# Kernel tuning notes

Hardware: AMD Instinct MI355X
Metric: run time of the kernel (lower is better)

The kernel has to match this reference:

```python
import jax, jax.numpy as jnp
import numpy as np

ALPHA = 0.2  # LeakyReLU negative slope
OUT_FEATURES = 64


def setup_inputs() -> dict:
    key = jax.random.key(0)
    k1, k2, k3, k4 = jax.random.split(key, 4)
    n_nodes, n_edges = 50000, 800000
    in_f, out_f, n_heads = 128, OUT_FEATURES, 4
    x = jax.random.normal(k1, (n_nodes, in_f), dtype=jnp.float32)
    edge_index = jax.random.randint(k2, (2, n_edges), 0, n_nodes, dtype=jnp.int64)
    # xavier-ish scaled params
    W = jax.random.normal(k3, (n_heads, in_f, out_f), dtype=jnp.float32) * (1.0 / np.sqrt(in_f))
    a = jax.random.normal(k4, (n_heads, 2 * out_f, 1), dtype=jnp.float32) * (1.0 / np.sqrt(2 * out_f))
    return {"x": x, "edge_index": edge_index, "W": W, "a": a}


def reference(x, edge_index, W, a):
    n_nodes = x.shape[0]
    out_f = W.shape[-1]
    src, dst = edge_index[0], edge_index[1]
    # per-head linear transform: (n, h, o)
    xt = jnp.einsum('ni,hio->nho', x, W)
    x_src = xt[src]  # (e, h, o) - edge-wise gather
    x_dst = xt[dst]
    # split attention vector: concat([x_src, x_dst]) @ a == x_src@a_src + x_dst@a_dst
    a_src = a[:, :out_f, 0]  # (h, o)
    a_dst = a[:, out_f:, 0]
    e = jnp.einsum('eho,ho->eh', x_src, a_src) + jnp.einsum('eho,ho->eh', x_dst, a_dst)
    e = jax.nn.leaky_relu(e, negative_slope=ALPHA)
    # segment softmax over incoming edges of each dst node (all heads at once)
    max_e = jax.ops.segment_max(e, dst, num_segments=n_nodes)  # (n, h), -inf for empty
    max_e = jnp.where(max_e == -jnp.inf, 0.0, max_e)
    exp_e = jnp.exp(e - max_e[dst])
    sum_exp = jax.ops.segment_sum(exp_e, dst, num_segments=n_nodes)
    attention = exp_e / (sum_exp[dst] + 1e-10)  # (e, h)
    # weighted scatter-add aggregation
    weighted = x_src * attention[..., None]  # (e, h, o)
    out = jax.ops.segment_sum(weighted, dst, num_segments=n_nodes)  # (n, h, o)
    out = out.reshape(n_nodes, -1)  # concat heads
    return out
```

## Files before the change

kernel.cpp:

```cpp
#include <hip/hip_runtime.h>
#include <math.h>

constexpr int IN_F  = 128;
constexpr int OUT_F = 64;
constexpr int HEADS = 4;
constexpr int COLS  = HEADS * OUT_F;
constexpr float ALPHA = 0.2f;
constexpr int CAP  = 64;
constexpr int NBUCK = 256;
constexpr int REPL  = 8;
constexpr int CAPBR = 768;
constexpr int CH_A  = 3840;
constexpr float QS   = 7.0f / 127.0f;
constexpr float QINV = 127.0f / 7.0f;

typedef __attribute__((ext_vector_type(8))) short short8v;
typedef __attribute__((ext_vector_type(4))) float f32x4;

__device__ inline unsigned short f2bf(float f) {
  unsigned int u = __float_as_uint(f);
  u += 0x7FFF + ((u >> 16) & 1);
  return (unsigned short)(u >> 16);
}

__device__ inline int wave_incl_scan(int v, int lane) {
  #pragma unroll
  for (int ofs = 1; ofs < 64; ofs <<= 1) {
    int tv = __shfl_up(v, ofs, 64);
    if (lane >= ofs) v += tv;
  }
  return v;
}

__device__ inline void fma8u(float* acc, float p, const uint2 v) {
  acc[0] += p * (float)( v.x        & 0xFF);
  acc[1] += p * (float)((v.x >> 8 ) & 0xFF);
  acc[2] += p * (float)((v.x >> 16) & 0xFF);
  acc[3] += p * (float)( v.x >> 24        );
  acc[4] += p * (float)( v.y        & 0xFF);
  acc[5] += p * (float)((v.y >> 8 ) & 0xFF);
  acc[6] += p * (float)((v.y >> 16) & 0xFF);
  acc[7] += p * (float)( v.y >> 24        );
}

__global__ __launch_bounds__(256) void k_prep(const float* __restrict__ W,
                                              unsigned short* __restrict__ Wb,
                                              int* __restrict__ gcursorR) {
  int i = blockIdx.x * 256 + threadIdx.x;
  if (i < NBUCK * REPL) gcursorR[i] = 0;
  if (i < HEADS * IN_F * OUT_F) {
    int h = i >> 13;
    int o = (i >> 7) & 63;
    int k = i & 127;
    Wb[i] = f2bf(W[(size_t)h * 8192 + k * 64 + o]);
  }
}

__global__ __launch_bounds__(256) void k_big(const float* __restrict__ x,
                                             const unsigned short* __restrict__ Wb,
                                             const float* __restrict__ a,
                                             const int* __restrict__ ei,
                                             unsigned char* __restrict__ xtb8,
                                             float* __restrict__ s_src,
                                             float* __restrict__ s_dst,
                                             int* __restrict__ gcursorR,
                                             unsigned int* __restrict__ gbuf,
                                             int n, int E, int NB_A) {
  __shared__ char smem[19456];
  __shared__ int wt[4];
  const int bid = blockIdx.x;
  const int t = threadIdx.x;
  const int lane = t & 63;
  const int wid = t >> 6;

  if (bid < NB_A) {
    unsigned int* stage = (unsigned int*)smem;
    int* cnt   = (int*)(smem + 15360);
    int* basei = (int*)(smem + 16384);
    int* cur   = (int*)(smem + 17408);
    int* gbase = (int*)(smem + 18432);
    const int rep = bid & (REPL - 1);

    cnt[t] = 0;
    __syncthreads();

    const int e0 = bid * CH_A;
    for (int i = t; i < CH_A; i += 256) {
      int e = e0 + i;
      if (e < E) atomicAdd(&cnt[ei[E + e] >> 8], 1);
    }
    __syncthreads();

    {
      int v = cnt[t];
      int incl = wave_incl_scan(v, lane);
      if (lane == 63) wt[wid] = incl;
      __syncthreads();
      int wofs = 0;
      #pragma unroll
      for (int w = 0; w < 4; ++w) wofs += (w < wid) ? wt[w] : 0;
      basei[t] = wofs + incl - v;
      cur[t] = wofs + incl - v;
    }
    __syncthreads();

    for (int i = t; i < CH_A; i += 256) {
      int e = e0 + i;
      if (e < E) {
        int src = ei[e];
        int dst = ei[E + e];
        int b = dst >> 8;
        int pos = atomicAdd(&cur[b], 1);
        stage[pos] = ((unsigned int)src << 16) | (unsigned int)(dst & 255);
      }
    }
    __syncthreads();

    if (t < NBUCK) {
      int c = cnt[t];
      gbase[t] = c ? atomicAdd(&gcursorR[t * REPL + rep], c) : 0;
    }
    __syncthreads();

    for (int b = wid; b < NBUCK; b += 4) {
      int c = cnt[b];
      int gb = gbase[b];
      int lb = basei[b];
      unsigned int* gdst = gbuf + ((size_t)b * REPL + rep) * CAPBR + gb;
      for (int i = lane; i < c; i += 64)
        gdst[i] = stage[lb + i];
    }
    return;
  }

  unsigned short* xls = (unsigned short*)smem;
  const int rbase = (bid - NB_A) * 64;
  const int w = wid;

  for (int c = t; c < 2048; c += 256) {
    int row = c >> 5;
    int i4  = c & 31;
    int grow = rbase + row;
    float4 v = make_float4(0.f, 0.f, 0.f, 0.f);
    if (grow < n) v = *(const float4*)(x + (size_t)grow * IN_F + i4 * 4);
    unsigned int p0 = (unsigned int)f2bf(v.x) | ((unsigned int)f2bf(v.y) << 16);
    unsigned int p1 = (unsigned int)f2bf(v.z) | ((unsigned int)f2bf(v.w) << 16);
    int byte = row * 256 + ((i4 * 8) ^ ((row & 7) << 4));
    *(uint2*)((char*)xls + byte) = make_uint2(p0, p1);
  }
  __syncthreads();

  const unsigned short* Wh = Wb + (size_t)w * 8192;
  const int nfix = lane & 15;
  const int kg   = lane >> 4;

  f32x4 acc[4][4] = {};

  #pragma unroll
  for (int kk = 0; kk < 4; ++kk) {
    short8v bfrag[4];
    #pragma unroll
    for (int ni = 0; ni < 4; ++ni)
      bfrag[ni] = *(const short8v*)(Wh + (ni * 16 + nfix) * 128 + kk * 32 + kg * 8);
    #pragma unroll
    for (int mi = 0; mi < 4; ++mi) {
      int m = mi * 16 + nfix;
      int abyte = m * 256 + ((kk * 64 + kg * 16) ^ ((m & 7) << 4));
      short8v afrag = *(const short8v*)((char*)xls + abyte);
      #pragma unroll
      for (int ni = 0; ni < 4; ++ni)
        acc[mi][ni] = __builtin_amdgcn_mfma_f32_16x16x32_bf16(
            afrag, bfrag[ni], acc[mi][ni], 0, 0, 0);
    }
  }

  float as[4], ad[4];
  #pragma unroll
  for (int ni = 0; ni < 4; ++ni) {
    as[ni] = a[w * 128 + ni * 16 + nfix];
    ad[ni] = a[w * 128 + 64 + ni * 16 + nfix];
  }
  #pragma unroll
  for (int mi = 0; mi < 4; ++mi) {
    #pragma unroll
    for (int r = 0; r < 4; ++r) {
      float ps = 0.f, pd = 0.f;
      #pragma unroll
      for (int ni = 0; ni < 4; ++ni) {
        ps += acc[mi][ni][r] * as[ni];
        pd += acc[mi][ni][r] * ad[ni];
      }
      #pragma unroll
      for (int m = 1; m < 16; m <<= 1) {
        ps += __shfl_xor(ps, m);
        pd += __shfl_xor(pd, m);
      }
      if ((lane & 15) == 0) {
        int row = rbase + mi * 16 + (kg << 2) + r;
        if (row < n) {
          s_src[(size_t)row * 4 + w] = ps;
          s_dst[(size_t)row * 4 + w] = pd;
        }
      }
    }
  }

  #pragma unroll
  for (int mi = 0; mi < 4; ++mi) {
    int row0 = rbase + mi * 16 + (kg << 2);
    #pragma unroll
    for (int r = 0; r < 4; ++r) {
      int row = row0 + r;
      if (row < n) {
        unsigned char* orow = xtb8 + (size_t)row * COLS + (w << 6) + nfix;
        #pragma unroll
        for (int ni = 0; ni < 4; ++ni) {
          float q = acc[mi][ni][r] * QINV;
          q = fminf(fmaxf(q, -127.f), 127.f);
          orow[ni * 16] = (unsigned char)((int)rintf(q) + 128);
        }
      }
    }
  }
}

__global__ __launch_bounds__(256) void k_binB(const unsigned int* __restrict__ gbuf,
                                              const int* __restrict__ gcursorR,
                                              unsigned short* __restrict__ csr16,
                                              int* __restrict__ deg, int n) {
  __shared__ int d2[256];
  const int b = blockIdx.x;
  const int t = threadIdx.x;
  d2[t] = 0;
  __syncthreads();

  #pragma unroll
  for (int r = 0; r < REPL; ++r) {
    const int cnt = gcursorR[b * REPL + r];
    const unsigned int* gp = gbuf + ((size_t)b * REPL + r) * CAPBR;
    for (int i = t; i < cnt; i += 256) {
      unsigned int en = gp[i];
      int dstLow = en & 255;
      int src = en >> 16;
      int rr = atomicAdd(&d2[dstLow], 1);
      if (rr < CAP) {
        int node = (b << 8) + dstLow;
        csr16[((size_t)node << 6) + rr] = (unsigned short)src;
      }
    }
  }
  __syncthreads();

  int node = (b << 8) + t;
  if (node < n) deg[node] = d2[t];
}

__global__ __launch_bounds__(128) void k_aggr(const unsigned short* __restrict__ csr16,
                                              const int* __restrict__ deg,
                                              const float* __restrict__ s_src,
                                              const float* __restrict__ s_dst,
                                              const unsigned char* __restrict__ xtb8,
                                              float* __restrict__ out, int n) {
  int node = (blockIdx.x * 128 + threadIdx.x) >> 6;
  if (node >= n) return;
  int lane = threadIdx.x & 63;
  int half = lane >> 5;
  int g    = lane & 31;
  int h    = g >> 3;
  int cb   = g << 3;

  int s    = node << 6;
  int d    = deg[node];
  if (d > CAP) d = CAP;
  int eEnd = s + d;
  float sd = s_dst[node * 4 + h];

  float acc[8] = {};
  float psum = 0.f;

  int j = s + half;
  while (j + 6 < eEnd) {
    int s0 = (int)csr16[j];
    int s1 = (int)csr16[j + 2];
    int s2 = (int)csr16[j + 4];
    int s3 = (int)csr16[j + 6];
    float sc0 = s_src[s0 * 4 + h];
    float sc1 = s_src[s1 * 4 + h];
    float sc2 = s_src[s2 * 4 + h];
    float sc3 = s_src[s3 * 4 + h];
    uint2 r0 = *(const uint2*)(xtb8 + ((size_t)s0 << 8) + cb);
    uint2 r1 = *(const uint2*)(xtb8 + ((size_t)s1 << 8) + cb);
    uint2 r2 = *(const uint2*)(xtb8 + ((size_t)s2 << 8) + cb);
    uint2 r3 = *(const uint2*)(xtb8 + ((size_t)s3 << 8) + cb);
    float v0 = sc0 + sd; v0 = v0 >= 0.f ? v0 : ALPHA * v0;
    float v1 = sc1 + sd; v1 = v1 >= 0.f ? v1 : ALPHA * v1;
    float v2 = sc2 + sd; v2 = v2 >= 0.f ? v2 : ALPHA * v2;
    float v3 = sc3 + sd; v3 = v3 >= 0.f ? v3 : ALPHA * v3;
    float p0 = __expf(v0);
    float p1 = __expf(v1);
    float p2 = __expf(v2);
    float p3 = __expf(v3);
    psum += (p0 + p1) + (p2 + p3);
    fma8u(acc, p0, r0);
    fma8u(acc, p1, r1);
    fma8u(acc, p2, r2);
    fma8u(acc, p3, r3);
    j += 8;
  }
  while (j < eEnd) {
    int s0 = (int)csr16[j];
    float sc0 = s_src[s0 * 4 + h];
    uint2 r0 = *(const uint2*)(xtb8 + ((size_t)s0 << 8) + cb);
    float v0 = sc0 + sd; v0 = v0 >= 0.f ? v0 : ALPHA * v0;
    float p0 = __expf(v0);
    psum += p0;
    fma8u(acc, p0, r0);
    j += 2;
  }

  psum += __shfl_xor(psum, 32);
  #pragma unroll
  for (int k = 0; k < 8; ++k) acc[k] += __shfl_xor(acc[k], 32);

  float inv = 1.f / (psum + 1e-10f);
  float biasc = 128.f * QS;
  float4 o;
  if (half) o = make_float4(acc[4] * inv * QS - biasc, acc[5] * inv * QS - biasc,
                            acc[6] * inv * QS - biasc, acc[7] * inv * QS - biasc);
  else      o = make_float4(acc[0] * inv * QS - biasc, acc[1] * inv * QS - biasc,
                            acc[2] * inv * QS - biasc, acc[3] * inv * QS - biasc);
  *(float4*)(out + (size_t)node * COLS + (g << 3) + half * 4) = o;
}

extern "C" void kernel_launch(void* const* d_in, const int* in_sizes, int n_in,
                              void* d_out, int out_size, void* d_ws, size_t ws_size,
                              hipStream_t stream) {
  const float* x  = (const float*)d_in[0];
  const int*   ei = (const int*)d_in[1];
  const float* W  = (const float*)d_in[2];
  const float* a  = (const float*)d_in[3];
  float* out = (float*)d_out;

  const int n = in_sizes[0] / IN_F;
  const int E = in_sizes[1] / 2;
  const int GB = (n + 63) / 64;
  const int NB_A = (E + CH_A - 1) / CH_A;
  const int NBKT = (n + 255) / 256;

  char* ws = (char*)d_ws;
  size_t off = 0;
  unsigned char* xtb8 = (unsigned char*)(ws + off); off += (size_t)n * COLS;
  unsigned short* Wb  = (unsigned short*)(ws + off); off += (size_t)HEADS * IN_F * OUT_F * 2;
  float* s_src = (float*)(ws + off);   off += (size_t)n * 4 * 4;
  float* s_dst = (float*)(ws + off);   off += (size_t)n * 4 * 4;
  int* deg = (int*)(ws + off);         off += (size_t)n * 4;
  int* gcursorR = (int*)(ws + off);    off += (size_t)NBUCK * REPL * 4;
  unsigned int* gbuf = (unsigned int*)(ws + off); off += (size_t)NBUCK * REPL * CAPBR * 4;
  unsigned short* csr16 = (unsigned short*)(ws + off); off += (size_t)n * CAP * 2;

  k_prep<<<128, 256, 0, stream>>>(W, Wb, gcursorR);

  k_big<<<NB_A + GB, 256, 0, stream>>>(x, Wb, a, ei, xtb8, s_src, s_dst,
                                       gcursorR, gbuf, n, E, NB_A);

  k_binB<<<NBKT, 256, 0, stream>>>(gbuf, gcursorR, csr16, deg, n);

  k_aggr<<<(n + 1) / 2, 128, 0, stream>>>(csr16, deg, s_src, s_dst, xtb8, out, n);
}
```

Measured before the change: 95.82 us.

## Fuse bucket-CSR build into main kernel via done counter; widen aggr loads

Folds the separate binning kernel into k_big as trailing blocks that spin on a global completion counter set by the edge-scatter blocks, which removes one kernel launch and lets the CSR build overlap the GEMM blocks. k_big also gets an occupancy hint via launch bounds. In k_aggr, each lane now loads 16 bytes per source row instead of 8 and four edge groups run per wave, which adds a two-step shuffle reduction. Spinning blocks rely on the producer blocks being scheduled first, which risks deadlock or wasted CU time if they are not.

```diff
diff --git a/kernel.cpp b/kernel.cpp
--- a/kernel.cpp
+++ b/kernel.cpp
@@ -32,22 +32,32 @@
   return v;
 }
 
-__device__ inline void fma8u(float* acc, float p, const uint2 v) {
-  acc[0] += p * (float)( v.x        & 0xFF);
-  acc[1] += p * (float)((v.x >> 8 ) & 0xFF);
-  acc[2] += p * (float)((v.x >> 16) & 0xFF);
-  acc[3] += p * (float)( v.x >> 24        );
-  acc[4] += p * (float)( v.y        & 0xFF);
-  acc[5] += p * (float)((v.y >> 8 ) & 0xFF);
-  acc[6] += p * (float)((v.y >> 16) & 0xFF);
-  acc[7] += p * (float)( v.y >> 24        );
+__device__ inline void fma16u(float* acc, float p, const uint4 v) {
+  acc[0]  += p * (float)( v.x        & 0xFF);
+  acc[1]  += p * (float)((v.x >> 8 ) & 0xFF);
+  acc[2]  += p * (float)((v.x >> 16) & 0xFF);
+  acc[3]  += p * (float)( v.x >> 24        );
+  acc[4]  += p * (float)( v.y        & 0xFF);
+  acc[5]  += p * (float)((v.y >> 8 ) & 0xFF);
+  acc[6]  += p * (float)((v.y >> 16) & 0xFF);
+  acc[7]  += p * (float)( v.y >> 24        );
+  acc[8]  += p * (float)( v.z        & 0xFF);
+  acc[9]  += p * (float)((v.z >> 8 ) & 0xFF);
+  acc[10] += p * (float)((v.z >> 16) & 0xFF);
+  acc[11] += p * (float)( v.z >> 24        );
+  acc[12] += p * (float)( v.w        & 0xFF);
+  acc[13] += p * (float)((v.w >> 8 ) & 0xFF);
+  acc[14] += p * (float)((v.w >> 16) & 0xFF);
+  acc[15] += p * (float)( v.w >> 24        );
 }
 
 __global__ __launch_bounds__(256) void k_prep(const float* __restrict__ W,
                                               unsigned short* __restrict__ Wb,
-                                              int* __restrict__ gcursorR) {
+                                              int* __restrict__ gcursorR,
+                                              int* __restrict__ done) {
   int i = blockIdx.x * 256 + threadIdx.x;
   if (i < NBUCK * REPL) gcursorR[i] = 0;
+  if (i == 0) *done = 0;
   if (i < HEADS * IN_F * OUT_F) {
     int h = i >> 13;
     int o = (i >> 7) & 63;
@@ -56,16 +66,19 @@
   }
 }
 
-__global__ __launch_bounds__(256) void k_big(const float* __restrict__ x,
-                                             const unsigned short* __restrict__ Wb,
-                                             const float* __restrict__ a,
-                                             const int* __restrict__ ei,
-                                             unsigned char* __restrict__ xtb8,
-                                             float* __restrict__ s_src,
-                                             float* __restrict__ s_dst,
-                                             int* __restrict__ gcursorR,
-                                             unsigned int* __restrict__ gbuf,
-                                             int n, int E, int NB_A) {
+__global__ __launch_bounds__(256, 5) void k_big(const float* __restrict__ x,
+                                                const unsigned short* __restrict__ Wb,
+                                                const float* __restrict__ a,
+                                                const int* __restrict__ ei,
+                                                unsigned char* __restrict__ xtb8,
+                                                float* __restrict__ s_src,
+                                                float* __restrict__ s_dst,
+                                                int* __restrict__ gcursorR,
+                                                unsigned int* __restrict__ gbuf,
+                                                unsigned short* __restrict__ csr16,
+                                                int* __restrict__ deg,
+                                                int* __restrict__ done,
+                                                int n, int E, int NB_A, int GB) {
   __shared__ char smem[19456];
   __shared__ int wt[4];
   const int bid = blockIdx.x;
@@ -130,6 +143,45 @@
       for (int i = lane; i < c; i += 64)
         gdst[i] = stage[lb + i];
     }
+    __syncthreads();
+    if (t == 0) {
+      __threadfence();
+      atomicAdd(done, 1);
+    }
+    return;
+  }
+
+  if (bid >= NB_A + GB) {
+    int* d2 = (int*)smem;
+    const int b = bid - NB_A - GB;
+    if (t == 0) {
+      while (atomicAdd(done, 0) < NB_A) __builtin_amdgcn_s_sleep(8);
+    }
+    __syncthreads();
+    __threadfence();
+
+    d2[t] = 0;
+    __syncthreads();
+
+    #pragma unroll
+    for (int r = 0; r < REPL; ++r) {
+      const int cnt = gcursorR[b * REPL + r];
+      const unsigned int* gp = gbuf + ((size_t)b * REPL + r) * CAPBR;
+      for (int i = t; i < cnt; i += 256) {
+        unsigned int en = gp[i];
+        int dstLow = en & 255;
+        int src = en >> 16;
+        int rr = atomicAdd(&d2[dstLow], 1);
+        if (rr < CAP) {
+          int node = (b << 8) + dstLow;
+          csr16[((size_t)node << 6) + rr] = (unsigned short)src;
+        }
+      }
+    }
+    __syncthreads();
+
+    int node = (b << 8) + t;
+    if (node < n) deg[node] = d2[t];
     return;
   }
 
@@ -224,37 +276,6 @@
   }
 }
 
-__global__ __launch_bounds__(256) void k_binB(const unsigned int* __restrict__ gbuf,
-                                              const int* __restrict__ gcursorR,
-                                              unsigned short* __restrict__ csr16,
-                                              int* __restrict__ deg, int n) {
-  __shared__ int d2[256];
-  const int b = blockIdx.x;
-  const int t = threadIdx.x;
-  d2[t] = 0;
-  __syncthreads();
-
-  #pragma unroll
-  for (int r = 0; r < REPL; ++r) {
-    const int cnt = gcursorR[b * REPL + r];
-    const unsigned int* gp = gbuf + ((size_t)b * REPL + r) * CAPBR;
-    for (int i = t; i < cnt; i += 256) {
-      unsigned int en = gp[i];
-      int dstLow = en & 255;
-      int src = en >> 16;
-      int rr = atomicAdd(&d2[dstLow], 1);
-      if (rr < CAP) {
-        int node = (b << 8) + dstLow;
-        csr16[((size_t)node << 6) + rr] = (unsigned short)src;
-      }
-    }
-  }
-  __syncthreads();
-
-  int node = (b << 8) + t;
-  if (node < n) deg[node] = d2[t];
-}
-
 __global__ __launch_bounds__(128) void k_aggr(const unsigned short* __restrict__ csr16,
                                               const int* __restrict__ deg,
                                               const float* __restrict__ s_src,
@@ -264,10 +285,10 @@
   int node = (blockIdx.x * 128 + threadIdx.x) >> 6;
   if (node >= n) return;
   int lane = threadIdx.x & 63;
-  int half = lane >> 5;
-  int g    = lane & 31;
-  int h    = g >> 3;
-  int cb   = g << 3;
+  int grp  = lane >> 4;
+  int q    = lane & 15;
+  int h    = q >> 2;
+  int cb   = q << 4;
 
   int s    = node << 6;
   int d    = deg[node];
@@ -275,23 +296,23 @@
   int eEnd = s + d;
   float sd = s_dst[node * 4 + h];
 
-  float acc[8] = {};
+  float acc[16] = {};
   float psum = 0.f;
 
-  int j = s + half;
-  while (j + 6 < eEnd) {
+  int j = s + grp;
+  while (j + 12 < eEnd) {
     int s0 = (int)csr16[j];
-    int s1 = (int)csr16[j + 2];
-    int s2 = (int)csr16[j + 4];
-    int s3 = (int)csr16[j + 6];
+    int s1 = (int)csr16[j + 4];
+    int s2 = (int)csr16[j + 8];
+    int s3 = (int)csr16[j + 12];
     float sc0 = s_src[s0 * 4 + h];
     float sc1 = s_src[s1 * 4 + h];
     float sc2 = s_src[s2 * 4 + h];
     float sc3 = s_src[s3 * 4 + h];
-    uint2 r0 = *(const uint2*)(xtb8 + ((size_t)s0 << 8) + cb);
-    uint2 r1 = *(const uint2*)(xtb8 + ((size_t)s1 << 8) + cb);
-    uint2 r2 = *(const uint2*)(xtb8 + ((size_t)s2 << 8) + cb);
-    uint2 r3 = *(const uint2*)(xtb8 + ((size_t)s3 << 8) + cb);
+    uint4 r0 = *(const uint4*)(xtb8 + ((size_t)s0 << 8) + cb);
+    uint4 r1 = *(const uint4*)(xtb8 + ((size_t)s1 << 8) + cb);
+    uint4 r2 = *(const uint4*)(xtb8 + ((size_t)s2 << 8) + cb);
+    uint4 r3 = *(const uint4*)(xtb8 + ((size_t)s3 << 8) + cb);
     float v0 = sc0 + sd; v0 = v0 >= 0.f ? v0 : ALPHA * v0;
     float v1 = sc1 + sd; v1 = v1 >= 0.f ? v1 : ALPHA * v1;
     float v2 = sc2 + sd; v2 = v2 >= 0.f ? v2 : ALPHA * v2;
@@ -301,35 +322,38 @@
     float p2 = __expf(v2);
     float p3 = __expf(v3);
     psum += (p0 + p1) + (p2 + p3);
-    fma8u(acc, p0, r0);
-    fma8u(acc, p1, r1);
-    fma8u(acc, p2, r2);
-    fma8u(acc, p3, r3);
-    j += 8;
+    fma16u(acc, p0, r0);
+    fma16u(acc, p1, r1);
+    fma16u(acc, p2, r2);
+    fma16u(acc, p3, r3);
+    j += 16;
   }
   while (j < eEnd) {
     int s0 = (int)csr16[j];
     float sc0 = s_src[s0 * 4 + h];
-    uint2 r0 = *(const uint2*)(xtb8 + ((size_t)s0 << 8) + cb);
+    uint4 r0 = *(const uint4*)(xtb8 + ((size_t)s0 << 8) + cb);
     float v0 = sc0 + sd; v0 = v0 >= 0.f ? v0 : ALPHA * v0;
     float p0 = __expf(v0);
     psum += p0;
-    fma8u(acc, p0, r0);
-    j += 2;
-  }
-
+    fma16u(acc, p0, r0);
+    j += 4;
+  }
+
+  psum += __shfl_xor(psum, 16);
   psum += __shfl_xor(psum, 32);
   #pragma unroll
-  for (int k = 0; k < 8; ++k) acc[k] += __shfl_xor(acc[k], 32);
+  for (int k = 0; k < 16; ++k) {
+    acc[k] += __shfl_xor(acc[k], 16);
+    acc[k] += __shfl_xor(acc[k], 32);
+  }
 
   float inv = 1.f / (psum + 1e-10f);
   float biasc = 128.f * QS;
-  float4 o;
-  if (half) o = make_float4(acc[4] * inv * QS - biasc, acc[5] * inv * QS - biasc,
-                            acc[6] * inv * QS - biasc, acc[7] * inv * QS - biasc);
-  else      o = make_float4(acc[0] * inv * QS - biasc, acc[1] * inv * QS - biasc,
-                            acc[2] * inv * QS - biasc, acc[3] * inv * QS - biasc);
-  *(float4*)(out + (size_t)node * COLS + (g << 3) + half * 4) = o;
+  float4 o = make_float4(acc[grp * 4 + 0] * inv * QS - biasc,
+                         acc[grp * 4 + 1] * inv * QS - biasc,
+                         acc[grp * 4 + 2] * inv * QS - biasc,
+                         acc[grp * 4 + 3] * inv * QS - biasc);
+  *(float4*)(out + (size_t)node * COLS + (q << 4) + (grp << 2)) = o;
 }
 
 extern "C" void kernel_launch(void* const* d_in, const int* in_sizes, int n_in,
@@ -355,15 +379,15 @@
   float* s_dst = (float*)(ws + off);   off += (size_t)n * 4 * 4;
   int* deg = (int*)(ws + off);         off += (size_t)n * 4;
   int* gcursorR = (int*)(ws + off);    off += (size_t)NBUCK * REPL * 4;
+  int* done = (int*)(ws + off);        off += 256;
   unsigned int* gbuf = (unsigned int*)(ws + off); off += (size_t)NBUCK * REPL * CAPBR * 4;
   unsigned short* csr16 = (unsigned short*)(ws + off); off += (size_t)n * CAP * 2;
 
-  k_prep<<<128, 256, 0, stream>>>(W, Wb, gcursorR);
-
-  k_big<<<NB_A + GB, 256, 0, stream>>>(x, Wb, a, ei, xtb8, s_src, s_dst,
-                                       gcursorR, gbuf, n, E, NB_A);
-
-  k_binB<<<NBKT, 256, 0, stream>>>(gbuf, gcursorR, csr16, deg, n);
+  k_prep<<<128, 256, 0, stream>>>(W, Wb, gcursorR, done);
+
+  k_big<<<NB_A + GB + NBKT, 256, 0, stream>>>(x, Wb, a, ei, xtb8, s_src, s_dst,
+                                              gcursorR, gbuf, csr16, deg, done,
+                                              n, E, NB_A, GB);
 
   k_aggr<<<(n + 1) / 2, 128, 0, stream>>>(csr16, deg, s_src, s_dst, xtb8, out, n);
 }
```

Result: slower. 154.3 us (+61.0%).
